# Kernel tuning notes

Measured on AMD Instinct MI355X. Metric: run time of the kernel, lower is better.

Reference implementation:

```python
import jax, jax.numpy as jnp
import numpy as np

NUM_HEADS = 16
B, S, H = 2, 8192, 1024


def setup_inputs() -> dict:
    key = jax.random.key(0)
    ks = jax.random.split(key, 6)
    scale = 1.0 / np.sqrt(H)
    return {
        "hidden_states": jax.random.normal(ks[0], (B, S, H), dtype=jnp.float32),
        "Wq": jax.random.normal(ks[1], (H, H), dtype=jnp.float32) * scale,
        "Wk": jax.random.normal(ks[2], (H, H), dtype=jnp.float32) * scale,
        "Wv": jax.random.normal(ks[3], (H, H), dtype=jnp.float32) * scale,
        "Wg": jax.random.normal(ks[4], (H, H), dtype=jnp.float32) * scale,
        "Wo": jax.random.normal(ks[5], (H, H), dtype=jnp.float32) * scale,
        "gamma": jnp.ones((H,), dtype=jnp.float32),
        "beta": jnp.zeros((H,), dtype=jnp.float32),
    }


def reference(hidden_states, Wq, Wk, Wv, Wg, Wo, gamma, beta):
    b, s, h = hidden_states.shape
    nh = NUM_HEADS
    dk = h // nh
    dv = h // nh
    # projections (bias-free linears)
    q = (hidden_states @ Wq).reshape(b, s, nh, dk)
    k = (hidden_states @ Wk).reshape(b, s, nh, dk)
    v = (hidden_states @ Wv).reshape(b, s, nh, dv)
    g = hidden_states @ Wg  # [b, s, h]
    # elu+1 feature map
    q = jax.nn.elu(q) + 1.0
    k = jax.nn.elu(k) + 1.0
    # kv = k outer v per token, then contracted with q  ==> (q.k) * v (no [b,h,n,d,e] tensor)
    qk = jnp.sum(q * k, axis=-1, keepdims=True)        # [b, s, nh, 1]
    k_sum = jnp.sum(k, axis=1, keepdims=True)          # [b, 1, nh, dk] (global over seq)
    normalizer = jnp.sum(q * k_sum, axis=-1, keepdims=True)  # [b, s, nh, 1]
    z = qk * v / (normalizer + 1e-6)                   # [b, s, nh, dv]
    z = z.reshape(b, s, nh * dv)
    # LayerNorm (eps=1e-5, affine)
    mu = jnp.mean(z, axis=-1, keepdims=True)
    var = jnp.mean(jnp.square(z - mu), axis=-1, keepdims=True)
    z = (z - mu) * jax.lax.rsqrt(var + 1e-5) * gamma + beta
    # SiLU gating and output projection
    z = z * jax.nn.silu(g)
    return z @ Wo
```

## Files before the change

kernel.cpp:

```cpp
#include <hip/hip_runtime.h>


typedef unsigned short ushort_t;
typedef unsigned int uint_t;

using short8  = __attribute__((ext_vector_type(8))) short;
using floatx4 = __attribute__((ext_vector_type(4))) float;

#define HDIM  1024
#define T_TOK 16384
#define KSPLIT 3072

__device__ __forceinline__ ushort_t f2bf(float f) {
    uint_t u = __builtin_bit_cast(uint_t, f);
    u = (u + 0x7fff + ((u >> 16) & 1)) >> 16;
    return (ushort_t)u;
}
__device__ __forceinline__ float bf2f(ushort_t h) {
    uint_t u = ((uint_t)h) << 16;
    return __builtin_bit_cast(float, u);
}
__device__ __forceinline__ void split2(float f, ushort_t& hi, ushort_t& lo) {
    hi = f2bf(f);
    lo = f2bf(f - bf2f(hi));
}
__device__ __forceinline__ void gload_lds16(const ushort_t* g, ushort_t* l) {
    __builtin_amdgcn_global_load_lds(
        (const __attribute__((address_space(1))) void*)g,
        (__attribute__((address_space(3))) void*)l, 16, 0, 0);
}

__global__ void split_w(const float* __restrict__ W0, const float* __restrict__ W1,
                        const float* __restrict__ W2, const float* __restrict__ W3,
                        const float* __restrict__ W4, ushort_t* __restrict__ WT2) {
    __shared__ float tile[32][33];
    const int z = blockIdx.z;
    const float* W = (z == 0) ? W0 : (z == 1) ? W1 : (z == 2) ? W2 : (z == 3) ? W3 : W4;
    ushort_t* dst = WT2 + (size_t)z * HDIM * 2048;
    const int n0 = blockIdx.x * 32, k0 = blockIdx.y * 32;
    const int tx = threadIdx.x & 31, ty0 = threadIdx.x >> 5;
#pragma unroll
    for (int s = 0; s < 4; ++s) {
        int ty = ty0 + 8 * s;
        tile[ty][tx] = W[(size_t)(k0 + ty) * HDIM + n0 + tx];
    }
    __syncthreads();
#pragma unroll
    for (int s = 0; s < 4; ++s) {
        int ty = ty0 + 8 * s;
        float v = tile[tx][ty];
        ushort_t hi, lo;
        split2(v, hi, lo);
        dst[(size_t)(n0 + ty) * 2048 + k0 + tx] = hi;
        dst[(size_t)(n0 + ty) * 2048 + 1024 + k0 + tx] = lo;
    }
}

__global__ __launch_bounds__(256)
void split_hidden(const float* __restrict__ h, ushort_t* __restrict__ Hs) {
    const int t = blockIdx.x;
    const int c = threadIdx.x;
    const float4 x = ((const float4*)(h + (size_t)t * HDIM))[c];
    ushort_t hi[4], lo[4];
    split2(x.x, hi[0], lo[0]); split2(x.y, hi[1], lo[1]);
    split2(x.z, hi[2], lo[2]); split2(x.w, hi[3], lo[3]);
    ushort_t* row = Hs + (size_t)t * 2048;
    uint2 hp, lp;
    hp.x = (uint_t)hi[0] | ((uint_t)hi[1] << 16);
    hp.y = (uint_t)hi[2] | ((uint_t)hi[3] << 16);
    lp.x = (uint_t)lo[0] | ((uint_t)lo[1] << 16);
    lp.y = (uint_t)lo[2] | ((uint_t)lo[3] << 16);
    *(uint2*)(row + c * 4) = hp;
    *(uint2*)(row + 1024 + c * 4) = lp;
}


#define FENCE() asm volatile("" ::: "memory")
#define VMW4()  asm volatile("s_waitcnt vmcnt(4)" ::: "memory")

#define STG_A(t, h, bsel) do { \
    const int ka_ = ((t) * 64 >= 2048) ? ((t) * 64 - 2048) : ((t) * 64); \
    gload_lds16(Ag + (size_t)((h) * 128) * 2048 + ka_, \
                &As[(bsel) * 16384 + ((h) * 128 + w * 16) * 64]); \
    gload_lds16(Ag + (size_t)((h) * 128 + 8) * 2048 + ka_, \
                &As[(bsel) * 16384 + ((h) * 128 + w * 16 + 8) * 64]); \
  } while (0)

#define STG_B(t, h, bsel) do { \
    const int kb_ = ((t) * 64 >= 1024) ? ((t) * 64 - 1024) : ((t) * 64); \
    gload_lds16(Bg + (size_t)((h) * 128) * 2048 + kb_, \
                &Bs[(bsel) * 16384 + ((h) * 128 + w * 16) * 64]); \
    gload_lds16(Bg + (size_t)((h) * 128 + 8) * 2048 + kb_, \
                &Bs[(bsel) * 16384 + ((h) * 128 + w * 16 + 8) * 64]); \
  } while (0)

#define RD_A(dst, bsel, mb, kc) do { \
    const ushort_t* _pa = ((kc) ? Ar1 : Ar0) + (bsel) * 16384; \
    _Pragma("unroll") \
    for (int _i = 0; _i < 4; ++_i) \
        dst[_i] = *(const short8*)(_pa + ((mb) + _i) * 1024); \
  } while (0)

#define RD_B(dst, bsel, kc) do { \
    const ushort_t* _pb = ((kc) ? Br1 : Br0) + (bsel) * 16384; \
    _Pragma("unroll") \
    for (int _j = 0; _j < 4; ++_j) \
        dst[_j] = *(const short8*)(_pb + _j * 1024); \
  } while (0)

#define MMX(mb, a, b) do { \
    __builtin_amdgcn_s_setprio(1); \
    _Pragma("unroll") \
    for (int _i = 0; _i < 4; ++_i) \
    _Pragma("unroll") \
    for (int _j = 0; _j < 4; ++_j) \
        acc[(mb) + _i][_j] = __builtin_amdgcn_mfma_f32_16x16x32_bf16( \
            a[_i], b[_j], acc[(mb) + _i][_j], 0, 0, 0); \
    __builtin_amdgcn_s_setprio(0); \
  } while (0)

#define TILE(t, bsel) do { \
     \
    RD_A(afB, bsel, 4, 0); \
    STG_A((t) + 1, 0, (bsel) ^ 1); STG_A((t) + 1, 1, (bsel) ^ 1); \
    MMX(0, afA, bfv0); \
     \
    RD_A(afA, bsel, 0, 1); \
    RD_B(bfv1, bsel, 1); \
    MMX(4, afB, bfv0); \
     \
    RD_A(afB, bsel, 4, 1); \
    MMX(0, afA, bfv1); \
     \
    __builtin_amdgcn_sched_barrier(0); \
    asm volatile("s_waitcnt lgkmcnt(0)" ::: "memory"); \
    FENCE(); __builtin_amdgcn_s_barrier(); FENCE(); \
    STG_B((t) + 2, 0, bsel); STG_B((t) + 2, 1, bsel); \
    VMW4(); \
    FENCE(); __builtin_amdgcn_s_barrier(); FENCE(); \
    __builtin_amdgcn_sched_barrier(0); \
     \
    RD_A(afA, (bsel) ^ 1, 0, 0); \
    RD_B(bfv0, (bsel) ^ 1, 0); \
    MMX(4, afB, bfv1); \
  } while (0)

template <int EPI>
__global__ __launch_bounds__(512, 2)
void gemm256(const ushort_t* __restrict__ A, const ushort_t* __restrict__ Bw,
             float* __restrict__ D, const float* __restrict__ kf,
             const float* __restrict__ ksum, float* __restrict__ scbuf,
             ushort_t* __restrict__ zbuf, const float* __restrict__ gamma,
             const float* __restrict__ beta, float* __restrict__ partial) {
    __shared__ ushort_t As[2 * 256 * 64];
    __shared__ ushort_t Bs[2 * 256 * 64];
    const int tid = threadIdx.x;
    const int bx = blockIdx.x, by = blockIdx.y;
    const int w = tid >> 6, lane = tid & 63;
    const int wm = w & 1, wn = w >> 1;
    const int lrow = lane & 15, lq = lane >> 4;

    const int srow = lane >> 3;
    const int scol = ((lane & 7) ^ srow) * 8;
    const ushort_t* Ag = A + (size_t)(bx * 256 + w * 16 + srow) * 2048 + scol;
    const ushort_t* Bg = Bw + (size_t)(by * 256 + w * 16 + srow) * 2048 + scol;

    const int c0 = (lq ^ (lrow & 7)) * 8;
    const int c1 = ((lq + 4) ^ (lrow & 7)) * 8;
    const ushort_t* Ar0 = As + (wm * 128 + lrow) * 64 + c0;
    const ushort_t* Ar1 = As + (wm * 128 + lrow) * 64 + c1;
    const ushort_t* Br0 = Bs + (wn * 64 + lrow) * 64 + c0;
    const ushort_t* Br1 = Bs + (wn * 64 + lrow) * 64 + c1;

    floatx4 acc[8][4] = {};
    short8 afA[4], afB[4], bfv0[4], bfv1[4];

    STG_A(0, 0, 0); STG_A(0, 1, 0);
    STG_B(0, 0, 0); STG_B(0, 1, 0);
    STG_B(1, 0, 1); STG_B(1, 1, 1);
    VMW4();
    FENCE(); __builtin_amdgcn_s_barrier(); FENCE();
    __builtin_amdgcn_sched_barrier(0);
    RD_A(afA, 0, 0, 0);
    RD_B(bfv0, 0, 0);

#pragma unroll 1
    for (int t = 0; t < 48; t += 2) {
        TILE(t, 0);
        TILE(t + 1, 1);
    }

    const int rowbase = bx * 256 + wm * 128 + lq * 4;
    const int colbase = by * 256 + wn * 64 + lrow;

    if constexpr (EPI == 0) {
        float s[4] = {0.f, 0.f, 0.f, 0.f};
#pragma unroll
        for (int i = 0; i < 8; ++i)
#pragma unroll
            for (int j = 0; j < 4; ++j) {
                const int col = colbase + j * 16;
#pragma unroll
                for (int r = 0; r < 4; ++r) {
                    const int row = rowbase + i * 16 + r;
                    float val = acc[i][j][r];
                    val = (val > 0.0f) ? (val + 1.0f) : (expm1f(val) + 1.0f);
                    s[j] += val;
                    D[(size_t)row * HDIM + col] = val;
                }
            }
#pragma unroll
        for (int j = 0; j < 4; ++j) {
            s[j] += __shfl_xor(s[j], 16, 64);
            s[j] += __shfl_xor(s[j], 32, 64);
        }
        if (lq == 0) {
            const int g = bx * 2 + wm;
#pragma unroll
            for (int j = 0; j < 4; ++j)
                partial[(size_t)g * HDIM + colbase + j * 16] = s[j];
        }
    } else if constexpr (EPI == 2) {
#pragma unroll
        for (int i = 0; i < 8; ++i)
#pragma unroll
            for (int j = 0; j < 4; ++j) {
                const int col = colbase + j * 16;
#pragma unroll
                for (int r = 0; r < 4; ++r) {
                    const int row = rowbase + i * 16 + r;
                    D[(size_t)row * HDIM + col] = acc[i][j][r];
                }
            }
    } else if constexpr (EPI == 1) {
        const int b = bx >> 5;
        float ksv[4];
#pragma unroll
        for (int j = 0; j < 4; ++j) ksv[j] = ksum[b * HDIM + colbase + j * 16];
        const int h = by * 4 + wn;
#pragma unroll
        for (int i = 0; i < 8; ++i)
#pragma unroll
            for (int r = 0; r < 4; ++r) {
                const int row = rowbase + i * 16 + r;
                float qk = 0.f, nm = 0.f;
#pragma unroll
                for (int j = 0; j < 4; ++j) {
                    float qv = acc[i][j][r];
                    qv = (qv > 0.0f) ? (qv + 1.0f) : (expm1f(qv) + 1.0f);
                    const float kv = kf[(size_t)row * HDIM + colbase + j * 16];
                    qk += qv * kv;
                    nm += qv * ksv[j];
                }
#pragma unroll
                for (int off = 1; off < 16; off <<= 1) {
                    qk += __shfl_xor(qk, off, 64);
                    nm += __shfl_xor(nm, off, 64);
                }
                if (lrow == 0) scbuf[row * 16 + h] = qk / (nm + 1e-6f);
            }
    } else {
#pragma unroll
        for (int i = 0; i < 8; ++i)
#pragma unroll
            for (int j = 0; j < 4; ++j) {
                const int col = colbase + j * 16;
                const float gam = gamma[col], bet = beta[col];
#pragma unroll
                for (int r = 0; r < 4; ++r) {
                    const int row = rowbase + i * 16 + r;
                    ushort_t* zr = zbuf + (size_t)row * 2048;
                    const float zn = bf2f(zr[col]) + bf2f(zr[1024 + col]);
                    const float g = acc[i][j][r];
                    const float sg = g / (1.0f + expf(-g));
                    ushort_t hi, lo;
                    split2((zn * gam + bet) * sg, hi, lo);
                    zr[col] = hi;
                    zr[1024 + col] = lo;
                }
            }
    }
}

template <int EPI>
__global__ __launch_bounds__(256)
void gemm_swz(const ushort_t* __restrict__ A, const ushort_t* __restrict__ Bw,
              float* __restrict__ D, const float* __restrict__ kf,
              const float* __restrict__ ksum, float* __restrict__ scbuf,
              ushort_t* __restrict__ zbuf) {
    __shared__ ushort_t As[128 * 64];
    __shared__ ushort_t Bs[128 * 64];
    const int tid = threadIdx.x;
    const int bx = blockIdx.x, by = blockIdx.y;
    const int w = tid >> 6, lane = tid & 63;
    const int wm = w & 1, wn = w >> 1;
    const int lrow = lane & 15, lq = lane >> 4;

    const int srow = lane >> 3;
    const int scol = ((lane & 7) ^ srow) * 8;
    const ushort_t* Ag = A + (size_t)(bx * 128 + w * 32 + srow) * 2048 + scol;
    const ushort_t* Bg = Bw + (size_t)(by * 128 + w * 32 + srow) * 2048 + scol;

    floatx4 acc[4][4] = {};

    for (int k0 = 0; k0 < KSPLIT; k0 += 64) {
        const int ka = k0 - ((k0 >= 2048) ? 2048 : 0);
        const int kb = k0 - ((k0 >= 1024) ? 1024 : 0);
        __syncthreads();
#pragma unroll
        for (int n = 0; n < 4; ++n) {
            gload_lds16(Ag + (size_t)(n * 8) * 2048 + ka, &As[(w * 32 + n * 8) * 64]);
            gload_lds16(Bg + (size_t)(n * 8) * 2048 + kb, &Bs[(w * 32 + n * 8) * 64]);
        }
        __syncthreads();
#pragma unroll
        for (int kk = 0; kk < 64; kk += 32) {
            short8 af[4], bf[4];
#pragma unroll
            for (int i = 0; i < 4; ++i) {
                const int c = (((kk >> 3) + lq) ^ (lrow & 7)) * 8;
                af[i] = *(const short8*)&As[(wm * 64 + i * 16 + lrow) * 64 + c];
            }
#pragma unroll
            for (int j = 0; j < 4; ++j) {
                const int c = (((kk >> 3) + lq) ^ (lrow & 7)) * 8;
                bf[j] = *(const short8*)&Bs[(wn * 64 + j * 16 + lrow) * 64 + c];
            }
#pragma unroll
            for (int i = 0; i < 4; ++i)
#pragma unroll
                for (int j = 0; j < 4; ++j)
                    acc[i][j] = __builtin_amdgcn_mfma_f32_16x16x32_bf16(af[i], bf[j], acc[i][j], 0, 0, 0);
        }
    }

    const int rowbase = bx * 128 + wm * 64 + lq * 4;
    const int colbase = by * 128 + wn * 64 + lrow;
#pragma unroll
    for (int i = 0; i < 4; ++i)
#pragma unroll
        for (int j = 0; j < 4; ++j) {
            const int col = colbase + j * 16;
#pragma unroll
            for (int r = 0; r < 4; ++r) {
                const int row = rowbase + i * 16 + r;
                float val = acc[i][j][r];
                if (EPI == 0) val = (val > 0.0f) ? (val + 1.0f) : (expm1f(val) + 1.0f);
                D[(size_t)row * HDIM + col] = val;
            }
        }
}

__global__ void ksum_partial(const float* __restrict__ kf, float* __restrict__ partial) {
    const int rg = blockIdx.x;
    const int tid = threadIdx.x;
    const float4* p = (const float4*)(kf + (size_t)rg * 64 * HDIM) + tid;
    float4 s = {0.f, 0.f, 0.f, 0.f};
    for (int r = 0; r < 64; ++r) {
        float4 x = p[(size_t)r * (HDIM / 4)];
        s.x += x.x; s.y += x.y; s.z += x.z; s.w += x.w;
    }
    ((float4*)(partial + (size_t)rg * HDIM))[tid] = s;
}
template <int NG>
__global__ void ksum_reduce(const float* __restrict__ partial, float* __restrict__ ksum) {
    const int b = blockIdx.y;
    const int c = blockIdx.x * 256 + threadIdx.x;
    float s = 0.f;
    const float* p = partial + (size_t)b * NG * HDIM + c;
    for (int rg = 0; rg < NG; ++rg) s += p[(size_t)rg * HDIM];
    ksum[b * HDIM + c] = s;
}

__global__ __launch_bounds__(256)
void token_lite(float* vz, const float* __restrict__ scbuf) {
    const int t = blockIdx.x;
    const int tid = threadIdx.x;
    const float4 v = ((const float4*)(vz + (size_t)t * HDIM))[tid];
    const float sc = scbuf[t * 16 + (tid >> 4)];
    float z[4] = {v.x * sc, v.y * sc, v.z * sc, v.w * sc};

    __shared__ float red[8];
    const int wv = tid >> 6, lane = tid & 63;

    float s1 = z[0] + z[1] + z[2] + z[3];
#pragma unroll
    for (int off = 1; off < 64; off <<= 1) s1 += __shfl_xor(s1, off, 64);
    if (lane == 0) red[wv] = s1;
    __syncthreads();
    const float mu = (red[0] + red[1] + red[2] + red[3]) * (1.0f / 1024.0f);

    float d[4] = {z[0] - mu, z[1] - mu, z[2] - mu, z[3] - mu};
    float s2 = d[0] * d[0] + d[1] * d[1] + d[2] * d[2] + d[3] * d[3];
#pragma unroll
    for (int off = 1; off < 64; off <<= 1) s2 += __shfl_xor(s2, off, 64);
    __syncthreads();
    if (lane == 0) red[4 + wv] = s2;
    __syncthreads();
    const float var = (red[4] + red[5] + red[6] + red[7]) * (1.0f / 1024.0f);
    const float rstd = rsqrtf(var + 1e-5f);

    ushort_t* zrow = (ushort_t*)(vz + (size_t)t * HDIM);
    ushort_t hi[4], lo[4];
#pragma unroll
    for (int c = 0; c < 4; ++c) split2(d[c] * rstd, hi[c], lo[c]);
    uint2 hp, lp;
    hp.x = (uint_t)hi[0] | ((uint_t)hi[1] << 16);
    hp.y = (uint_t)hi[2] | ((uint_t)hi[3] << 16);
    lp.x = (uint_t)lo[0] | ((uint_t)lo[1] << 16);
    lp.y = (uint_t)lo[2] | ((uint_t)lo[3] << 16);
    *(uint2*)(zrow + tid * 4) = hp;
    *(uint2*)(zrow + 1024 + tid * 4) = lp;
}

template <int VAR>
__global__ __launch_bounds__(256, 2)
void gemm_split(const float* __restrict__ A,
                const ushort_t* __restrict__ B0, const ushort_t* __restrict__ B1,
                const ushort_t* __restrict__ B2,
                float* __restrict__ D0, float* __restrict__ D1, float* __restrict__ D2,
                int K) {
    __shared__ ushort_t Ah[128 * 72];
    __shared__ ushort_t Al[128 * 72];
    __shared__ ushort_t Bh[128 * 72];
    __shared__ ushort_t Bl[128 * 72];
    const int tid = threadIdx.x;
    const int bx = blockIdx.x, by = blockIdx.y;
    const ushort_t* Bt;
    float* D;
    int n0;
    bool act;
    if (VAR == 1) {
        const int wsel = by >> 3;
        Bt = (wsel == 0) ? B0 : (wsel == 1) ? B1 : B2;
        D = (wsel == 0) ? D0 : (wsel == 1) ? D1 : D2;
        n0 = (by & 7) * 128;
        act = (wsel == 0);
    } else {
        Bt = B0; D = D0; n0 = by * 128; act = true;
    }
    const int w = tid >> 6, lane = tid & 63;
    const int wm = w & 1, wn = w >> 1;
    const int lrow = lane & 15, lq = lane >> 4;
    const int srow = tid >> 1;
    const int shalf = (tid & 1) * 32;
    const float* Arow = A + (size_t)(bx * 128 + srow) * K;
    const ushort_t* Brow = Bt + (size_t)(n0 + srow) * 2048;
    floatx4 acc[4][4] = {};
    for (int k0 = 0; k0 < K; k0 += 64) {
        float4 afr[8];
        uint4 bhr[4], blr[4];
#pragma unroll
        for (int g = 0; g < 4; ++g) {
            afr[2 * g]     = *(const float4*)(Arow + k0 + shalf + g * 8);
            afr[2 * g + 1] = *(const float4*)(Arow + k0 + shalf + g * 8 + 4);
            bhr[g] = *(const uint4*)(Brow + k0 + shalf + g * 8);
            blr[g] = *(const uint4*)(Brow + 1024 + k0 + shalf + g * 8);
        }
        __syncthreads();
#pragma unroll
        for (int g = 0; g < 4; ++g) {
            ushort_t h[8], l[8];
            const float4 f0 = afr[2 * g], f1 = afr[2 * g + 1];
            split2(f0.x, h[0], l[0]); split2(f0.y, h[1], l[1]);
            split2(f0.z, h[2], l[2]); split2(f0.w, h[3], l[3]);
            split2(f1.x, h[4], l[4]); split2(f1.y, h[5], l[5]);
            split2(f1.z, h[6], l[6]); split2(f1.w, h[7], l[7]);
            uint4 hp, lp;
            hp.x = (uint_t)h[0] | ((uint_t)h[1] << 16);
            hp.y = (uint_t)h[2] | ((uint_t)h[3] << 16);
            hp.z = (uint_t)h[4] | ((uint_t)h[5] << 16);
            hp.w = (uint_t)h[6] | ((uint_t)h[7] << 16);
            lp.x = (uint_t)l[0] | ((uint_t)l[1] << 16);
            lp.y = (uint_t)l[2] | ((uint_t)l[3] << 16);
            lp.z = (uint_t)l[4] | ((uint_t)l[5] << 16);
            lp.w = (uint_t)l[6] | ((uint_t)l[7] << 16);
            *(uint4*)&Ah[srow * 72 + shalf + g * 8] = hp;
            *(uint4*)&Al[srow * 72 + shalf + g * 8] = lp;
            *(uint4*)&Bh[srow * 72 + shalf + g * 8] = bhr[g];
            *(uint4*)&Bl[srow * 72 + shalf + g * 8] = blr[g];
        }
        __syncthreads();
#pragma unroll
        for (int kk = 0; kk < 64; kk += 32) {
            short8 ah[4], bh[4], xl[4];
#pragma unroll
            for (int i = 0; i < 4; ++i)
                ah[i] = *(const short8*)&Ah[(wm * 64 + i * 16 + lrow) * 72 + kk + lq * 8];
#pragma unroll
            for (int j = 0; j < 4; ++j)
                bh[j] = *(const short8*)&Bh[(wn * 64 + j * 16 + lrow) * 72 + kk + lq * 8];
#pragma unroll
            for (int i = 0; i < 4; ++i)
#pragma unroll
                for (int j = 0; j < 4; ++j)
                    acc[i][j] = __builtin_amdgcn_mfma_f32_16x16x32_bf16(ah[i], bh[j], acc[i][j], 0, 0, 0);
#pragma unroll
            for (int i = 0; i < 4; ++i)
                xl[i] = *(const short8*)&Al[(wm * 64 + i * 16 + lrow) * 72 + kk + lq * 8];
#pragma unroll
            for (int i = 0; i < 4; ++i)
#pragma unroll
                for (int j = 0; j < 4; ++j)
                    acc[i][j] = __builtin_amdgcn_mfma_f32_16x16x32_bf16(xl[i], bh[j], acc[i][j], 0, 0, 0);
#pragma unroll
            for (int j = 0; j < 4; ++j)
                xl[j] = *(const short8*)&Bl[(wn * 64 + j * 16 + lrow) * 72 + kk + lq * 8];
#pragma unroll
            for (int i = 0; i < 4; ++i)
#pragma unroll
                for (int j = 0; j < 4; ++j)
                    acc[i][j] = __builtin_amdgcn_mfma_f32_16x16x32_bf16(ah[i], xl[j], acc[i][j], 0, 0, 0);
        }
    }
    const int rowbase = bx * 128 + wm * 64 + lq * 4;
    const int colbase = n0 + wn * 64 + lrow;
#pragma unroll
    for (int i = 0; i < 4; ++i)
#pragma unroll
        for (int j = 0; j < 4; ++j) {
            const int col = colbase + j * 16;
#pragma unroll
            for (int r = 0; r < 4; ++r) {
                const int row = rowbase + i * 16 + r;
                float val = acc[i][j][r];
                if (act) val = (val > 0.0f) ? (val + 1.0f) : (expm1f(val) + 1.0f);
                D[(size_t)row * HDIM + col] = val;
            }
        }
}

__global__ __launch_bounds__(256)
void token_f32(const float* __restrict__ qd, const float* __restrict__ vd,
               const float* __restrict__ gd, float* kz,
               const float* __restrict__ ksum,
               const float* __restrict__ gamma, const float* __restrict__ beta,
               int chunk_base) {
    const int tl = blockIdx.x;
    const int t = chunk_base + tl;
    const int b = t >> 13;
    const int tid = threadIdx.x;
    const float4 q = ((const float4*)(qd + (size_t)tl * HDIM))[tid];
    const float4 k = ((const float4*)(kz + (size_t)t * HDIM))[tid];
    const float4 v = ((const float4*)(vd + (size_t)tl * HDIM))[tid];
    const float4 ks = ((const float4*)(ksum + (size_t)b * HDIM))[tid];
    float qk = q.x * k.x + q.y * k.y + q.z * k.z + q.w * k.w;
    float nm = q.x * ks.x + q.y * ks.y + q.z * ks.z + q.w * ks.w;
#pragma unroll
    for (int off = 1; off < 16; off <<= 1) {
        qk += __shfl_xor(qk, off, 64);
        nm += __shfl_xor(nm, off, 64);
    }
    const float sc = qk / (nm + 1e-6f);
    float z[4] = {v.x * sc, v.y * sc, v.z * sc, v.w * sc};
    __shared__ float red[8];
    const int wv = tid >> 6, lane = tid & 63;
    float s1 = z[0] + z[1] + z[2] + z[3];
#pragma unroll
    for (int off = 1; off < 64; off <<= 1) s1 += __shfl_xor(s1, off, 64);
    if (lane == 0) red[wv] = s1;
    __syncthreads();
    const float mu = (red[0] + red[1] + red[2] + red[3]) * (1.0f / 1024.0f);
    float d[4] = {z[0] - mu, z[1] - mu, z[2] - mu, z[3] - mu};
    float s2 = d[0] * d[0] + d[1] * d[1] + d[2] * d[2] + d[3] * d[3];
#pragma unroll
    for (int off = 1; off < 64; off <<= 1) s2 += __shfl_xor(s2, off, 64);
    __syncthreads();
    if (lane == 0) red[4 + wv] = s2;
    __syncthreads();
    const float var = (red[4] + red[5] + red[6] + red[7]) * (1.0f / 1024.0f);
    const float rstd = rsqrtf(var + 1e-5f);
    const float4 gm = ((const float4*)gamma)[tid];
    const float4 bt = ((const float4*)beta)[tid];
    const float4 g = ((const float4*)(gd + (size_t)tl * HDIM))[tid];
    const float gv[4] = {g.x, g.y, g.z, g.w};
    const float gmv[4] = {gm.x, gm.y, gm.z, gm.w};
    const float btv[4] = {bt.x, bt.y, bt.z, bt.w};
    ushort_t hi[4], lo[4];
#pragma unroll
    for (int c = 0; c < 4; ++c) {
        const float zn = d[c] * rstd * gmv[c] + btv[c];
        const float sg = gv[c] / (1.0f + expf(-gv[c]));
        split2(zn * sg, hi[c], lo[c]);
    }
    ushort_t* zrow = (ushort_t*)(kz + (size_t)t * HDIM);
    uint2 hp, lp;
    hp.x = (uint_t)hi[0] | ((uint_t)hi[1] << 16);
    hp.y = (uint_t)hi[2] | ((uint_t)hi[3] << 16);
    lp.x = (uint_t)lo[0] | ((uint_t)lo[1] << 16);
    lp.y = (uint_t)lo[2] | ((uint_t)lo[3] << 16);
    *(uint2*)(zrow + tid * 4) = hp;
    *(uint2*)(zrow + 1024 + tid * 4) = lp;
}

extern "C" void kernel_launch(void* const* d_in, const int* in_sizes, int n_in,
                              void* d_out, int out_size, void* d_ws, size_t ws_size,
                              hipStream_t stream) {
    const float* hidden = (const float*)d_in[0];
    const float* Wq = (const float*)d_in[1];
    const float* Wk = (const float*)d_in[2];
    const float* Wv = (const float*)d_in[3];
    const float* Wg = (const float*)d_in[4];
    const float* Wo = (const float*)d_in[5];
    const float* gamma = (const float*)d_in[6];
    const float* beta = (const float*)d_in[7];

    char* w = (char*)d_ws;
    float* kb = (float*)w;            w += (size_t)67108864;
    ushort_t* WT2 = (ushort_t*)w;     w += (size_t)20971520;
    float* partial = (float*)w;       w += (size_t)1048576;
    float* ksum = (float*)w;          w += (size_t)8192;
    float* scbuf = (float*)w;         w += (size_t)1048576;
    const size_t base = (size_t)(w - (char*)d_ws);

    ushort_t* Wk2 = WT2;
    ushort_t* Wq2 = WT2 + (size_t)1 * HDIM * 2048;
    ushort_t* Wv2 = WT2 + (size_t)2 * HDIM * 2048;
    ushort_t* Wg2 = WT2 + (size_t)3 * HDIM * 2048;
    ushort_t* Wo2 = WT2 + (size_t)4 * HDIM * 2048;

    split_w<<<dim3(32, 32, 5), 256, 0, stream>>>(Wk, Wq, Wv, Wg, Wo, WT2);

    if (ws_size >= base + 67108864ull) {
        ushort_t* Hs = (ushort_t*)w;
        split_hidden<<<dim3(T_TOK), 256, 0, stream>>>(hidden, Hs);
        gemm256<0><<<dim3(64, 4), 512, 0, stream>>>(Hs, Wk2, kb, nullptr, nullptr,
                                                    nullptr, nullptr, nullptr, nullptr,
                                                    partial);
        ksum_reduce<64><<<dim3(4, 2), 256, 0, stream>>>(partial, ksum);
        gemm256<1><<<dim3(64, 4), 512, 0, stream>>>(Hs, Wq2, nullptr, kb, ksum,
                                                    scbuf, nullptr, nullptr, nullptr,
                                                    nullptr);
        gemm256<2><<<dim3(64, 4), 512, 0, stream>>>(Hs, Wv2, kb, nullptr, nullptr,
                                                    nullptr, nullptr, nullptr, nullptr,
                                                    nullptr);
        token_lite<<<dim3(T_TOK), 256, 0, stream>>>(kb, scbuf);
        gemm256<3><<<dim3(64, 4), 512, 0, stream>>>(Hs, Wg2, nullptr, nullptr, nullptr,
                                                    nullptr, (ushort_t*)kb, gamma, beta,
                                                    nullptr);
        gemm256<2><<<dim3(64, 4), 512, 0, stream>>>((const ushort_t*)kb, Wo2,
                                                    (float*)d_out, nullptr, nullptr,
                                                    nullptr, nullptr, nullptr, nullptr,
                                                    nullptr);
    } else {
        const int C = 2048;
        float* qc = (float*)w;
        float* vc = qc + (size_t)C * HDIM;
        float* gc = vc + (size_t)C * HDIM;
        gemm_split<0><<<dim3(128, 8), 256, 0, stream>>>(hidden, Wk2, nullptr, nullptr,
                                                        kb, nullptr, nullptr, HDIM);
        ksum_partial<<<dim3(256), 256, 0, stream>>>(kb, partial);
        ksum_reduce<128><<<dim3(4, 2), 256, 0, stream>>>(partial, ksum);
        for (int c = 0; c < 8; ++c) {
            const float* Ac = hidden + (size_t)c * C * HDIM;
            gemm_split<1><<<dim3(C / 128, 24), 256, 0, stream>>>(Ac, Wq2, Wv2, Wg2,
                                                                 qc, vc, gc, HDIM);
            token_f32<<<dim3(C), 256, 0, stream>>>(qc, vc, gc, kb, ksum,
                                                   gamma, beta, c * C);
        }
        gemm_swz<2><<<dim3(128, 8), 256, 0, stream>>>((const ushort_t*)kb, Wo2,
                                                      (float*)d_out, nullptr, nullptr,
                                                      nullptr, nullptr);
    }
}
```

Measured before the change: 663.9 us.

## Shrink GEMM tiles to 256x128 with K=32 and 256-thread blocks

Reworks the bf16 split GEMM kernel from 256x256 output tiles with 512 threads and a K=64 step to 256x128 tiles with 256 threads and a K=32 step. The launch grid doubles along N, and the LDS footprint shrinks accordingly. The staggered prefetch, where B was staged two tiles ahead, becomes a plain double buffer with a full vmcnt(0) wait each step. The aim is more, lighter blocks per CU and better latency hiding. The risks are lower operand reuse per tile, more barriers per unit of K, and less overlap between loads and MFMA.

```diff
diff --git a/kernel.cpp b/kernel.cpp
--- a/kernel.cpp
+++ b/kernel.cpp
@@ -76,36 +76,35 @@
 
 
 #define FENCE() asm volatile("" ::: "memory")
-#define VMW4()  asm volatile("s_waitcnt vmcnt(4)" ::: "memory")
-
-#define STG_A(t, h, bsel) do { \
-    const int ka_ = ((t) * 64 >= 2048) ? ((t) * 64 - 2048) : ((t) * 64); \
-    gload_lds16(Ag + (size_t)((h) * 128) * 2048 + ka_, \
-                &As[(bsel) * 16384 + ((h) * 128 + w * 16) * 64]); \
-    gload_lds16(Ag + (size_t)((h) * 128 + 8) * 2048 + ka_, \
-                &As[(bsel) * 16384 + ((h) * 128 + w * 16 + 8) * 64]); \
+
+#define STG_A4(t, bsel) do { \
+    const int ka_ = ((t) * 32 >= 2048) ? ((t) * 32 - 2048) : ((t) * 32); \
+    _Pragma("unroll") \
+    for (int _g = 0; _g < 4; ++_g) \
+        gload_lds16(Ag + (size_t)(_g * 16) * 2048 + ka_, \
+                    &As[(bsel) * 8192 + (w * 64 + _g * 16) * 32]); \
   } while (0)
 
-#define STG_B(t, h, bsel) do { \
-    const int kb_ = ((t) * 64 >= 1024) ? ((t) * 64 - 1024) : ((t) * 64); \
-    gload_lds16(Bg + (size_t)((h) * 128) * 2048 + kb_, \
-                &Bs[(bsel) * 16384 + ((h) * 128 + w * 16) * 64]); \
-    gload_lds16(Bg + (size_t)((h) * 128 + 8) * 2048 + kb_, \
-                &Bs[(bsel) * 16384 + ((h) * 128 + w * 16 + 8) * 64]); \
+#define STG_B2(t, bsel) do { \
+    const int kb_ = ((t) * 32 >= 1024) ? ((t) * 32 - 1024) : ((t) * 32); \
+    _Pragma("unroll") \
+    for (int _g = 0; _g < 2; ++_g) \
+        gload_lds16(Bg + (size_t)(_g * 16) * 2048 + kb_, \
+                    &Bs[(bsel) * 4096 + (w * 32 + _g * 16) * 32]); \
   } while (0)
 
-#define RD_A(dst, bsel, mb, kc) do { \
-    const ushort_t* _pa = ((kc) ? Ar1 : Ar0) + (bsel) * 16384; \
+#define RD_A(dst, bsel, mb) do { \
+    const ushort_t* _pa = Ar + (bsel) * 8192; \
     _Pragma("unroll") \
     for (int _i = 0; _i < 4; ++_i) \
-        dst[_i] = *(const short8*)(_pa + ((mb) + _i) * 1024); \
+        dst[_i] = *(const short8*)(_pa + ((mb) + _i) * 512); \
   } while (0)
 
-#define RD_B(dst, bsel, kc) do { \
-    const ushort_t* _pb = ((kc) ? Br1 : Br0) + (bsel) * 16384; \
+#define RD_B(dst, bsel) do { \
+    const ushort_t* _pb = Br + (bsel) * 4096; \
     _Pragma("unroll") \
     for (int _j = 0; _j < 4; ++_j) \
-        dst[_j] = *(const short8*)(_pb + _j * 1024); \
+        dst[_j] = *(const short8*)(_pb + _j * 512); \
   } while (0)
 
 #define MMX(mb, a, b) do { \
@@ -119,79 +118,64 @@
     __builtin_amdgcn_s_setprio(0); \
   } while (0)
 
-#define TILE(t, bsel) do { \
-     \
-    RD_A(afB, bsel, 4, 0); \
-    STG_A((t) + 1, 0, (bsel) ^ 1); STG_A((t) + 1, 1, (bsel) ^ 1); \
-    MMX(0, afA, bfv0); \
-     \
-    RD_A(afA, bsel, 0, 1); \
-    RD_B(bfv1, bsel, 1); \
-    MMX(4, afB, bfv0); \
-     \
-    RD_A(afB, bsel, 4, 1); \
-    MMX(0, afA, bfv1); \
-     \
+#define TILE32(t, bsel) do { \
+    RD_A(afB, bsel, 4); \
+    STG_A4((t) + 1, (bsel) ^ 1); \
+    MMX(0, afA, bfv); \
+    STG_B2((t) + 1, (bsel) ^ 1); \
+    MMX(4, afB, bfv); \
     __builtin_amdgcn_sched_barrier(0); \
     asm volatile("s_waitcnt lgkmcnt(0)" ::: "memory"); \
     FENCE(); __builtin_amdgcn_s_barrier(); FENCE(); \
-    STG_B((t) + 2, 0, bsel); STG_B((t) + 2, 1, bsel); \
-    VMW4(); \
+    asm volatile("s_waitcnt vmcnt(0)" ::: "memory"); \
     FENCE(); __builtin_amdgcn_s_barrier(); FENCE(); \
     __builtin_amdgcn_sched_barrier(0); \
-     \
-    RD_A(afA, (bsel) ^ 1, 0, 0); \
-    RD_B(bfv0, (bsel) ^ 1, 0); \
-    MMX(4, afB, bfv1); \
+    RD_A(afA, (bsel) ^ 1, 0); \
+    RD_B(bfv, (bsel) ^ 1); \
   } while (0)
 
 template <int EPI>
-__global__ __launch_bounds__(512, 2)
+__global__ __launch_bounds__(256)
 void gemm256(const ushort_t* __restrict__ A, const ushort_t* __restrict__ Bw,
              float* __restrict__ D, const float* __restrict__ kf,
              const float* __restrict__ ksum, float* __restrict__ scbuf,
              ushort_t* __restrict__ zbuf, const float* __restrict__ gamma,
              const float* __restrict__ beta, float* __restrict__ partial) {
-    __shared__ ushort_t As[2 * 256 * 64];
-    __shared__ ushort_t Bs[2 * 256 * 64];
+    __shared__ ushort_t As[2 * 256 * 32];
+    __shared__ ushort_t Bs[2 * 128 * 32];
     const int tid = threadIdx.x;
     const int bx = blockIdx.x, by = blockIdx.y;
     const int w = tid >> 6, lane = tid & 63;
     const int wm = w & 1, wn = w >> 1;
     const int lrow = lane & 15, lq = lane >> 4;
 
-    const int srow = lane >> 3;
-    const int scol = ((lane & 7) ^ srow) * 8;
-    const ushort_t* Ag = A + (size_t)(bx * 256 + w * 16 + srow) * 2048 + scol;
-    const ushort_t* Bg = Bw + (size_t)(by * 256 + w * 16 + srow) * 2048 + scol;
-
-    const int c0 = (lq ^ (lrow & 7)) * 8;
-    const int c1 = ((lq + 4) ^ (lrow & 7)) * 8;
-    const ushort_t* Ar0 = As + (wm * 128 + lrow) * 64 + c0;
-    const ushort_t* Ar1 = As + (wm * 128 + lrow) * 64 + c1;
-    const ushort_t* Br0 = Bs + (wn * 64 + lrow) * 64 + c0;
-    const ushort_t* Br1 = Bs + (wn * 64 + lrow) * 64 + c1;
+    const int srow = lane >> 2;
+    const int schunk = ((lane & 3) ^ (srow & 3)) * 8;
+    const ushort_t* Ag = A + (size_t)(bx * 256 + w * 64 + srow) * 2048 + schunk;
+    const ushort_t* Bg = Bw + (size_t)(by * 128 + w * 32 + srow) * 2048 + schunk;
+
+    const ushort_t* Ar = As + (wm * 128 + lrow) * 32 + ((lq ^ (lrow & 3)) * 8);
+    const ushort_t* Br = Bs + (wn * 64 + lrow) * 32 + ((lq ^ (lrow & 3)) * 8);
 
     floatx4 acc[8][4] = {};
-    short8 afA[4], afB[4], bfv0[4], bfv1[4];
-
-    STG_A(0, 0, 0); STG_A(0, 1, 0);
-    STG_B(0, 0, 0); STG_B(0, 1, 0);
-    STG_B(1, 0, 1); STG_B(1, 1, 1);
-    VMW4();
+    short8 afA[4], afB[4], bfv[4];
+
+    STG_A4(0, 0);
+    STG_B2(0, 0);
+    asm volatile("s_waitcnt vmcnt(0)" ::: "memory");
     FENCE(); __builtin_amdgcn_s_barrier(); FENCE();
     __builtin_amdgcn_sched_barrier(0);
-    RD_A(afA, 0, 0, 0);
-    RD_B(bfv0, 0, 0);
+    RD_A(afA, 0, 0);
+    RD_B(bfv, 0);
 
 #pragma unroll 1
-    for (int t = 0; t < 48; t += 2) {
-        TILE(t, 0);
-        TILE(t + 1, 1);
+    for (int t = 0; t < 96; t += 2) {
+        TILE32(t, 0);
+        TILE32(t + 1, 1);
     }
 
     const int rowbase = bx * 256 + wm * 128 + lq * 4;
-    const int colbase = by * 256 + wn * 64 + lrow;
+    const int colbase = by * 128 + wn * 64 + lrow;
 
     if constexpr (EPI == 0) {
         float s[4] = {0.f, 0.f, 0.f, 0.f};
@@ -237,7 +221,7 @@
         float ksv[4];
 #pragma unroll
         for (int j = 0; j < 4; ++j) ksv[j] = ksum[b * HDIM + colbase + j * 16];
-        const int h = by * 4 + wn;
+        const int h = by * 2 + wn;
 #pragma unroll
         for (int i = 0; i < 8; ++i)
 #pragma unroll
@@ -624,21 +608,21 @@
     if (ws_size >= base + 67108864ull) {
         ushort_t* Hs = (ushort_t*)w;
         split_hidden<<<dim3(T_TOK), 256, 0, stream>>>(hidden, Hs);
-        gemm256<0><<<dim3(64, 4), 512, 0, stream>>>(Hs, Wk2, kb, nullptr, nullptr,
+        gemm256<0><<<dim3(64, 8), 256, 0, stream>>>(Hs, Wk2, kb, nullptr, nullptr,
                                                     nullptr, nullptr, nullptr, nullptr,
                                                     partial);
         ksum_reduce<64><<<dim3(4, 2), 256, 0, stream>>>(partial, ksum);
-        gemm256<1><<<dim3(64, 4), 512, 0, stream>>>(Hs, Wq2, nullptr, kb, ksum,
+        gemm256<1><<<dim3(64, 8), 256, 0, stream>>>(Hs, Wq2, nullptr, kb, ksum,
                                                     scbuf, nullptr, nullptr, nullptr,
                                                     nullptr);
-        gemm256<2><<<dim3(64, 4), 512, 0, stream>>>(Hs, Wv2, kb, nullptr, nullptr,
+        gemm256<2><<<dim3(64, 8), 256, 0, stream>>>(Hs, Wv2, kb, nullptr, nullptr,
                                                     nullptr, nullptr, nullptr, nullptr,
                                                     nullptr);
         token_lite<<<dim3(T_TOK), 256, 0, stream>>>(kb, scbuf);
-        gemm256<3><<<dim3(64, 4), 512, 0, stream>>>(Hs, Wg2, nullptr, nullptr, nullptr,
+        gemm256<3><<<dim3(64, 8), 256, 0, stream>>>(Hs, Wg2, nullptr, nullptr, nullptr,
                                                     nullptr, (ushort_t*)kb, gamma, beta,
                                                     nullptr);
-        gemm256<2><<<dim3(64, 4), 512, 0, stream>>>((const ushort_t*)kb, Wo2,
+        gemm256<2><<<dim3(64, 8), 256, 0, stream>>>((const ushort_t*)kb, Wo2,
                                                     (float*)d_out, nullptr, nullptr,
                                                     nullptr, nullptr, nullptr, nullptr,
                                                     nullptr);
```

Result: slower. 1.284 ms (+93.4%).

## Add dedicated 256x128 double-buffered GEMM kernel for V projection

Applied to the files above, without the earlier changes.

Replaces the generic 256x256 gemm256 launch for the V projection with a new gemm_v kernel. It uses 256-thread blocks with 256x128 tiles, K-step 32, double-buffered LDS with direct global-to-LDS loads, and launch bounds allowing two blocks per CU. The aim is higher occupancy and better overlap of loads with MFMA work for this one GEMM. In exchange the kernel adds more code, uses smaller tiles that reload more data, and relies on hand-scheduled waits and barriers.

```diff
diff --git a/kernel.cpp b/kernel.cpp
--- a/kernel.cpp
+++ b/kernel.cpp
@@ -280,6 +280,104 @@
                 }
             }
     }
+}
+
+
+#define VSTG_A4(t, bsel) do { \
+    const int ka_ = ((t) * 32 >= 2048) ? ((t) * 32 - 2048) : ((t) * 32); \
+    _Pragma("unroll") \
+    for (int _g = 0; _g < 4; ++_g) \
+        gload_lds16(Ag + (size_t)(_g * 16) * 2048 + ka_, \
+                    &As[(bsel) * 8192 + (w * 64 + _g * 16) * 32]); \
+  } while (0)
+
+#define VSTG_B2(t, bsel) do { \
+    const int kb_ = ((t) * 32 >= 1024) ? ((t) * 32 - 1024) : ((t) * 32); \
+    _Pragma("unroll") \
+    for (int _g = 0; _g < 2; ++_g) \
+        gload_lds16(Bg + (size_t)(_g * 16) * 2048 + kb_, \
+                    &Bs[(bsel) * 4096 + (w * 32 + _g * 16) * 32]); \
+  } while (0)
+
+#define VRD_A(dst, bsel, mb) do { \
+    const ushort_t* _pa = Ar + (bsel) * 8192; \
+    _Pragma("unroll") \
+    for (int _i = 0; _i < 4; ++_i) \
+        dst[_i] = *(const short8*)(_pa + ((mb) + _i) * 512); \
+  } while (0)
+
+#define VRD_B(dst, bsel) do { \
+    const ushort_t* _pb = Br + (bsel) * 4096; \
+    _Pragma("unroll") \
+    for (int _j = 0; _j < 4; ++_j) \
+        dst[_j] = *(const short8*)(_pb + _j * 512); \
+  } while (0)
+
+#define VTILE32(t, bsel) do { \
+    VRD_A(afB, bsel, 4); \
+    VSTG_A4((t) + 1, (bsel) ^ 1); \
+    MMX(0, afA, bfv); \
+    VSTG_B2((t) + 1, (bsel) ^ 1); \
+    MMX(4, afB, bfv); \
+    __builtin_amdgcn_sched_barrier(0); \
+    asm volatile("s_waitcnt lgkmcnt(0)" ::: "memory"); \
+    FENCE(); __builtin_amdgcn_s_barrier(); FENCE(); \
+    asm volatile("s_waitcnt vmcnt(0)" ::: "memory"); \
+    FENCE(); __builtin_amdgcn_s_barrier(); FENCE(); \
+    __builtin_amdgcn_sched_barrier(0); \
+    VRD_A(afA, (bsel) ^ 1, 0); \
+    VRD_B(bfv, (bsel) ^ 1); \
+  } while (0)
+
+__global__ __launch_bounds__(256, 2)
+void gemm_v(const ushort_t* __restrict__ A, const ushort_t* __restrict__ Bw,
+            float* __restrict__ D) {
+    __shared__ ushort_t As[2 * 256 * 32];
+    __shared__ ushort_t Bs[2 * 128 * 32];
+    const int tid = threadIdx.x;
+    const int bx = blockIdx.x, by = blockIdx.y;
+    const int w = tid >> 6, lane = tid & 63;
+    const int wm = w & 1, wn = w >> 1;
+    const int lrow = lane & 15, lq = lane >> 4;
+
+    const int srow = lane >> 2;
+    const int schunk = ((lane & 3) ^ ((srow >> 1) & 3)) * 8;
+    const ushort_t* Ag = A + (size_t)(bx * 256 + w * 64 + srow) * 2048 + schunk;
+    const ushort_t* Bg = Bw + (size_t)(by * 128 + w * 32 + srow) * 2048 + schunk;
+
+    const ushort_t* Ar = As + (wm * 128 + lrow) * 32 + ((lq ^ ((lrow >> 1) & 3)) * 8);
+    const ushort_t* Br = Bs + (wn * 64 + lrow) * 32 + ((lq ^ ((lrow >> 1) & 3)) * 8);
+
+    floatx4 acc[8][4] = {};
+    short8 afA[4], afB[4], bfv[4];
+
+    VSTG_A4(0, 0);
+    VSTG_B2(0, 0);
+    asm volatile("s_waitcnt vmcnt(0)" ::: "memory");
+    FENCE(); __builtin_amdgcn_s_barrier(); FENCE();
+    __builtin_amdgcn_sched_barrier(0);
+    VRD_A(afA, 0, 0);
+    VRD_B(bfv, 0);
+
+#pragma unroll 1
+    for (int t = 0; t < 96; t += 2) {
+        VTILE32(t, 0);
+        VTILE32(t + 1, 1);
+    }
+
+    const int rowbase = bx * 256 + wm * 128 + lq * 4;
+    const int colbase = by * 128 + wn * 64 + lrow;
+#pragma unroll
+    for (int i = 0; i < 8; ++i)
+#pragma unroll
+        for (int j = 0; j < 4; ++j) {
+            const int col = colbase + j * 16;
+#pragma unroll
+            for (int r = 0; r < 4; ++r) {
+                const int row = rowbase + i * 16 + r;
+                D[(size_t)row * HDIM + col] = acc[i][j][r];
+            }
+        }
 }
 
 template <int EPI>
@@ -631,9 +729,7 @@
         gemm256<1><<<dim3(64, 4), 512, 0, stream>>>(Hs, Wq2, nullptr, kb, ksum,
                                                     scbuf, nullptr, nullptr, nullptr,
                                                     nullptr);
-        gemm256<2><<<dim3(64, 4), 512, 0, stream>>>(Hs, Wv2, kb, nullptr, nullptr,
-                                                    nullptr, nullptr, nullptr, nullptr,
-                                                    nullptr);
+        gemm_v<<<dim3(64, 8), 256, 0, stream>>>(Hs, Wv2, kb);
         token_lite<<<dim3(T_TOK), 256, 0, stream>>>(kb, scbuf);
         gemm256<3><<<dim3(64, 4), 512, 0, stream>>>(Hs, Wg2, nullptr, nullptr, nullptr,
                                                     nullptr, (ushort_t*)kb, gamma, beta,
```

Measured after the change: 855.8 us. 1.29x slower.
